# Performance work log

Measured on AMD Instinct MI355X. Metric: run time of the kernel, lower is better.

The kernel has to match this reference:

```python
import jax, jax.numpy as jnp
import numpy as np

N_NODES = 50000   # total nodes across the batch of graphs
N_EDGES = 800000  # avg degree 16
F_IN = 128        # num_features
DIM = 256         # hidden dim
N_LAYERS = 3      # num_gc_layers
N_GRAPHS = 512    # graphs in the batch (max(batch)+1)
BN_EPS = 1e-5


def setup_inputs() -> dict:
    key = jax.random.key(0)
    ks = jax.random.split(key, 16)
    inp = {}
    inp["x"] = jax.random.normal(ks[0], (N_NODES, F_IN), dtype=jnp.float32)
    inp["edge_index"] = jax.random.randint(ks[1], (2, N_EDGES), 0, N_NODES, dtype=jnp.int64)
    inp["batch"] = jnp.sort(jax.random.randint(ks[2], (N_NODES,), 0, N_GRAPHS, dtype=jnp.int64))
    k = 3
    for i in range(N_LAYERS):
        fin = F_IN if i == 0 else DIM
        inp[f"w1_{i}"] = jax.random.normal(ks[k], (fin, DIM), dtype=jnp.float32) / np.sqrt(fin); k += 1
        inp[f"b1_{i}"] = jnp.zeros((DIM,), dtype=jnp.float32)
        inp[f"w2_{i}"] = jax.random.normal(ks[k], (DIM, DIM), dtype=jnp.float32) / np.sqrt(DIM); k += 1
        inp[f"b2_{i}"] = jnp.zeros((DIM,), dtype=jnp.float32)
        inp[f"bn_g{i}"] = jnp.ones((DIM,), dtype=jnp.float32)
        inp[f"bn_b{i}"] = jnp.zeros((DIM,), dtype=jnp.float32)
    return inp


def _gin_layer(h, src, dst, w1, b1, w2, b2, g, b):
    # GINConv (eps=0): agg_i = h_i + sum_{j->i} h_j  (scatter-add over edges)
    agg = h + jax.ops.segment_sum(h[src], dst, num_segments=N_NODES)
    # MLP: Linear -> ReLU -> Linear
    m = jnp.maximum(agg @ w1 + b1, 0.0) @ w2 + b2
    # F.relu then BatchNorm1d (training mode: batch statistics, biased var)
    m = jnp.maximum(m, 0.0)
    mu = m.mean(axis=0)
    var = ((m - mu) ** 2).mean(axis=0)
    return g * (m - mu) / jnp.sqrt(var + BN_EPS) + b


def reference(x, edge_index, batch,
              w1_0, b1_0, w2_0, b2_0, bn_g0, bn_b0,
              w1_1, b1_1, w2_1, b2_1, bn_g1, bn_b1,
              w1_2, b1_2, w2_2, b2_2, bn_g2, bn_b2):
    src, dst = edge_index[0], edge_index[1]
    params = [
        (w1_0, b1_0, w2_0, b2_0, bn_g0, bn_b0),
        (w1_1, b1_1, w2_1, b2_1, bn_g1, bn_b1),
        (w1_2, b1_2, w2_2, b2_2, bn_g2, bn_b2),
    ]
    xs = []
    h = x
    for p in params:
        h = _gin_layer(h, src, dst, *p)
        xs.append(h)
    # global add-pool readout per layer, concat along feature dim
    pooled = jnp.concatenate(
        [jax.ops.segment_sum(hi, batch, num_segments=N_GRAPHS) for hi in xs], axis=1)
    return pooled, jnp.concatenate(xs, axis=1)
```

## Files before the change

kernel.cpp:

```cpp
#include <hip/hip_runtime.h>

#define N_NODES 50000
#define N_EDGES 800000
#define F_IN 128
#define DIM 256
#define N_GRAPHS 512
#define BN_EPS 1e-5f

typedef unsigned short u16;
typedef unsigned int u32;
using floatx4 = __attribute__((ext_vector_type(4))) float;
using short8 = __attribute__((ext_vector_type(8))) short;
using half2v = __attribute__((ext_vector_type(2))) _Float16;

#if __has_builtin(__builtin_amdgcn_fdot2)
#define HAS_FDOT2 1
#endif

__device__ __forceinline__ u16 f2h(float f) {
    _Float16 h = (_Float16)f;
    return __builtin_bit_cast(u16, h);
}
__device__ __forceinline__ float hlo(u32 u) {
    half2v h = __builtin_bit_cast(half2v, u);
    return (float)h.x;
}
__device__ __forceinline__ float hhi(u32 u) {
    half2v h = __builtin_bit_cast(half2v, u);
    return (float)h.y;
}
__device__ __forceinline__ u32 pack2(float a, float b) {
    half2v h = {(_Float16)a, (_Float16)b};
    return __builtin_bit_cast(u32, h);
}
__device__ __forceinline__ void dacc(u32 w, float& a, float& b) {
#ifdef HAS_FDOT2
    half2v v = __builtin_bit_cast(half2v, w);
    const half2v L = {(_Float16)1.0f, (_Float16)0.0f};
    const half2v Hm = {(_Float16)0.0f, (_Float16)1.0f};
    a = __builtin_amdgcn_fdot2(v, L, a, false);
    b = __builtin_amdgcn_fdot2(v, Hm, b, false);
#else
    a += hlo(w);
    b += hhi(w);
#endif
}
__device__ __forceinline__ void load_lds16(const void* g, void* l) {
    __builtin_amdgcn_global_load_lds((const __attribute__((address_space(1))) void*)g,
                                     (__attribute__((address_space(3))) void*)l, 16, 0, 0);
}


__global__ void count_deg(const int* __restrict__ dst, int* __restrict__ deg, int nE) {
    int e = blockIdx.x * 256 + threadIdx.x;
    if (e < nE) atomicAdd(&deg[dst[e]], 1);
}

__global__ void scan_block(const int* __restrict__ deg, int* __restrict__ row_start,
                           int* __restrict__ bsum, int n) {
    __shared__ int wtot[4];
    int i = blockIdx.x * 256 + threadIdx.x;
    int lane = threadIdx.x & 63, w = threadIdx.x >> 6;
    int v = (i < n) ? deg[i] : 0;
    int s = v;
#pragma unroll
    for (int d = 1; d < 64; d <<= 1) {
        int t = __shfl_up(s, d);
        if (lane >= d) s += t;
    }
    if (lane == 63) wtot[w] = s;
    __syncthreads();
    int off = 0;
#pragma unroll
    for (int k = 0; k < 4; ++k)
        if (k < w) off += wtot[k];
    s += off;
    if (i < n) row_start[i + 1] = s;
    if (threadIdx.x == 255) bsum[blockIdx.x] = s;
}

__global__ void scan_partials(const int* __restrict__ bsum, int* __restrict__ boff,
                              int* __restrict__ row_start, int* __restrict__ cursor, int nb) {
    __shared__ int wtot[4];
    int i = threadIdx.x;
    int lane = i & 63, w = i >> 6;
    int v = (i < nb) ? bsum[i] : 0;
    int s = v;
#pragma unroll
    for (int d = 1; d < 64; d <<= 1) {
        int t = __shfl_up(s, d);
        if (lane >= d) s += t;
    }
    if (lane == 63) wtot[w] = s;
    __syncthreads();
    int off = 0;
#pragma unroll
    for (int k = 0; k < 4; ++k)
        if (k < w) off += wtot[k];
    boff[i] = s + off - v;
    if (i == 0) { row_start[0] = 0; cursor[0] = 0; }
}

__global__ void add_offsets(int* __restrict__ row_start, int* __restrict__ cursor,
                            const int* __restrict__ boff, int n) {
    int i = blockIdx.x * 256 + threadIdx.x;
    if (i < n) {
        int fin = row_start[i + 1] + boff[blockIdx.x];
        row_start[i + 1] = fin;
        cursor[i + 1] = fin;
    }
}

__global__ void fill_csr(const int* __restrict__ src, const int* __restrict__ dst,
                         int* __restrict__ cursor, int* __restrict__ srcs, int nE) {
    int e = blockIdx.x * 256 + threadIdx.x;
    if (e < nE) {
        int p = atomicAdd(&cursor[dst[e]], 1);
        srcs[p] = src[e];
    }
}


__global__ void convert_all(const float4* __restrict__ x4, uint2* __restrict__ Hout, int n4,
                            const float* __restrict__ w10, const float* __restrict__ w11,
                            const float* __restrict__ w12, const float* __restrict__ w20,
                            const float* __restrict__ w21, const float* __restrict__ w22,
                            u16* __restrict__ Wall) {
    int i = blockIdx.x * 256 + threadIdx.x;
    if (i < n4) {
        float4 v = x4[i];
        uint2 p;
        p.x = pack2(v.x, v.y);
        p.y = pack2(v.z, v.w);
        Hout[i] = p;
        return;
    }
    int j = i - n4;
    if (j >= 360448) return;
    const float* w;
    int K, base;
    if (j < 32768)       { w = w10; K = 128; base = 0; }
    else if (j < 98304)  { w = w11; K = 256; base = 32768; }
    else if (j < 163840) { w = w12; K = 256; base = 98304; }
    else if (j < 229376) { w = w20; K = 256; base = 163840; }
    else if (j < 294912) { w = w21; K = 256; base = 229376; }
    else                 { w = w22; K = 256; base = 294912; }
    int loc = j - base;
    int nn = loc / K, kk = loc - nn * K;
    Wall[j] = f2h(w[(size_t)kk * 256 + nn]);
}


template <int K>
__global__ __launch_bounds__(256) void aggregate_v2(
    const u16* __restrict__ h, const int* __restrict__ row_start,
    const int* __restrict__ srcs, u16* __restrict__ outp, int n) {
    constexpr int RW = K / 2;
    constexpr int NSUB = (K == 256) ? 2 : 4;
    int node = (int)(((size_t)blockIdx.x * blockDim.x + threadIdx.x) >> 6);
    int lane = threadIdx.x & 63;
    if (node >= n) return;
    const u32* hb = (const u32*)h;
    const int sub = lane / (64 / NSUB);
    const int li = lane % (64 / NSUB);

    float acc[8];
#pragma unroll
    for (int t = 0; t < 8; ++t) acc[t] = 0.f;
    {
        if (sub == 0) {
            uint4 v = *(const uint4*)(hb + (size_t)node * RW + li * 4);
            dacc(v.x, acc[0], acc[1]);
            dacc(v.y, acc[2], acc[3]);
            dacc(v.z, acc[4], acc[5]);
            dacc(v.w, acc[6], acc[7]);
        }
    }

    int s = row_start[node], e = row_start[node + 1];
    for (int j0 = s; j0 < e; j0 += 64) {
        int myidx = (j0 + lane < e) ? srcs[j0 + lane] : 0;
        int cnt = min(64, e - j0);
        int j = 0;
        for (; j + NSUB * 8 - 1 < cnt; j += NSUB * 8) {
            uint4 g[8];
#pragma unroll
            for (int q = 0; q < 8; ++q) {
                int sq = __shfl(myidx, j + q * NSUB + sub);
                g[q] = *(const uint4*)(hb + (size_t)sq * RW + li * 4);
            }
#pragma unroll
            for (int q = 0; q < 8; ++q) {
                dacc(g[q].x, acc[0], acc[1]);
                dacc(g[q].y, acc[2], acc[3]);
                dacc(g[q].z, acc[4], acc[5]);
                dacc(g[q].w, acc[6], acc[7]);
            }
        }
        for (; j + NSUB * 4 - 1 < cnt; j += NSUB * 4) {
            uint4 g[4];
#pragma unroll
            for (int q = 0; q < 4; ++q) {
                int sq = __shfl(myidx, j + q * NSUB + sub);
                g[q] = *(const uint4*)(hb + (size_t)sq * RW + li * 4);
            }
#pragma unroll
            for (int q = 0; q < 4; ++q) {
                dacc(g[q].x, acc[0], acc[1]);
                dacc(g[q].y, acc[2], acc[3]);
                dacc(g[q].z, acc[4], acc[5]);
                dacc(g[q].w, acc[6], acc[7]);
            }
        }
        for (; j < cnt; j += NSUB) {
            int idx = j + sub;
            bool valid = idx < cnt;
            int sq = __shfl(myidx, valid ? idx : j);
            if (valid) {
                uint4 g = *(const uint4*)(hb + (size_t)sq * RW + li * 4);
                dacc(g.x, acc[0], acc[1]);
                dacc(g.y, acc[2], acc[3]);
                dacc(g.z, acc[4], acc[5]);
                dacc(g.w, acc[6], acc[7]);
            }
        }
    }

    if (NSUB == 4) {
#pragma unroll
        for (int t = 0; t < 8; ++t) acc[t] += __shfl_xor(acc[t], 16);
    }
#pragma unroll
    for (int t = 0; t < 8; ++t) acc[t] += __shfl_xor(acc[t], 32);

    if (sub == 0) {
        uint4 o;
        o.x = pack2(acc[0], acc[1]);
        o.y = pack2(acc[2], acc[3]);
        o.z = pack2(acc[4], acc[5]);
        o.w = pack2(acc[6], acc[7]);
        *(uint4*)((u32*)outp + (size_t)node * RW + li * 4) = o;
    }
}


template <int K1>
__global__ __launch_bounds__(512, 4) void mlp_fused(
    const u16* __restrict__ A, const u16* __restrict__ B1t, const float* __restrict__ b1,
    const u16* __restrict__ B2t, const float* __restrict__ b2,
    u16* __restrict__ Cout, float* __restrict__ sums, int M) {
    __shared__ u16 As[64 * 32];
    __shared__ u16 Bs[256 * 32];
    __shared__ u16 Ts[64 * 256];
    const int tid = threadIdx.x;
    const int w = tid >> 6, lane = tid & 63;
    const int wm = w >> 2, wn = w & 3;
    const int r = lane & 15, rg = lane >> 4;
    const int bm = blockIdx.x * 64;

    floatx4 acc[2][4];
#pragma unroll
    for (int i = 0; i < 2; ++i)
#pragma unroll
        for (int j = 0; j < 4; ++j) acc[i][j] = (floatx4){0.f, 0.f, 0.f, 0.f};

    for (int k0 = 0; k0 < K1; k0 += 32) {
        __syncthreads();
        if (tid < 256) {
            int arow = bm + (tid >> 2);
            if (arow >= M) arow = M - 1;
            load_lds16(A + (size_t)arow * K1 + k0 + (tid & 3) * 8, As + w * 512);
        }
#pragma unroll
        for (int q = 0; q < 2; ++q) {
            int i = q * 512 + tid;
            load_lds16(B1t + (size_t)(i >> 2) * K1 + k0 + (i & 3) * 8, Bs + (q * 8 + w) * 512);
        }
        __syncthreads();
        short8 a[2], b[4];
#pragma unroll
        for (int mi = 0; mi < 2; ++mi)
            a[mi] = *(const short8*)(As + (wm * 32 + mi * 16 + r) * 32 + rg * 8);
#pragma unroll
        for (int ni = 0; ni < 4; ++ni)
            b[ni] = *(const short8*)(Bs + (wn * 64 + ni * 16 + r) * 32 + rg * 8);
#pragma unroll
        for (int mi = 0; mi < 2; ++mi)
#pragma unroll
            for (int ni = 0; ni < 4; ++ni)
                acc[mi][ni] = __builtin_amdgcn_mfma_f32_16x16x32_f16(a[mi], b[ni], acc[mi][ni], 0, 0, 0);
    }
#pragma unroll
    for (int ni = 0; ni < 4; ++ni) {
        int col = wn * 64 + ni * 16 + r;
        float bv = b1[col];
#pragma unroll
        for (int mi = 0; mi < 2; ++mi)
#pragma unroll
            for (int rr = 0; rr < 4; ++rr) {
                int lrow = wm * 32 + mi * 16 + rg * 4 + rr;
                float v = fmaxf(acc[mi][ni][rr] + bv, 0.f);
                int chunk = (col >> 3) ^ (lrow & 7);
                *(u16*)((char*)Ts + lrow * 512 + chunk * 16 + (col & 7) * 2) = f2h(v);
            }
#pragma unroll
        for (int mi = 0; mi < 2; ++mi) acc[mi][ni] = (floatx4){0.f, 0.f, 0.f, 0.f};
    }

    for (int k0 = 0; k0 < 256; k0 += 32) {
        __syncthreads();
#pragma unroll
        for (int q = 0; q < 2; ++q) {
            int i = q * 512 + tid;
            load_lds16(B2t + (size_t)(i >> 2) * 256 + k0 + (i & 3) * 8, Bs + (q * 8 + w) * 512);
        }
        __syncthreads();
        short8 a[2], b[4];
#pragma unroll
        for (int mi = 0; mi < 2; ++mi) {
            int lrow = wm * 32 + mi * 16 + r;
            int chunk = ((k0 >> 3) + rg) ^ (lrow & 7);
            a[mi] = *(const short8*)((const char*)Ts + lrow * 512 + chunk * 16);
        }
#pragma unroll
        for (int ni = 0; ni < 4; ++ni)
            b[ni] = *(const short8*)(Bs + (wn * 64 + ni * 16 + r) * 32 + rg * 8);
#pragma unroll
        for (int mi = 0; mi < 2; ++mi)
#pragma unroll
            for (int ni = 0; ni < 4; ++ni)
                acc[mi][ni] = __builtin_amdgcn_mfma_f32_16x16x32_f16(a[mi], b[ni], acc[mi][ni], 0, 0, 0);
    }

#pragma unroll
    for (int ni = 0; ni < 4; ++ni) {
        int col = wn * 64 + ni * 16 + r;
        float bv = b2[col];
        float s = 0.f, s2 = 0.f;
#pragma unroll
        for (int mi = 0; mi < 2; ++mi)
#pragma unroll
            for (int rr = 0; rr < 4; ++rr) {
                int row = bm + wm * 32 + mi * 16 + rg * 4 + rr;
                if (row < M) {
                    float v = fmaxf(acc[mi][ni][rr] + bv, 0.f);
                    u16 qb = f2h(v);
                    float vq = hlo((u32)qb);
                    Cout[(size_t)row * 256 + col] = qb;
                    s += vq;
                    s2 += vq * vq;
                }
            }
        s += __shfl_xor(s, 16);
        s += __shfl_xor(s, 32);
        s2 += __shfl_xor(s2, 16);
        s2 += __shfl_xor(s2, 32);
        if (rg == 0) {
            atomicAdd(&sums[col], s);
            atomicAdd(&sums[256 + col], s2);
        }
    }
}


template <int WRITE_H>
__global__ void bn_apply_pool(const u16* __restrict__ Mb, const float* __restrict__ sums,
                              const float* __restrict__ g, const float* __restrict__ bb,
                              const int* __restrict__ batch, float* __restrict__ out_nodes,
                              u16* __restrict__ H, float* __restrict__ pooled,
                              int col_off, int n, float inv_n) {
    int w = threadIdx.x >> 6, lane = threadIdx.x & 63;
    int base = blockIdx.x * 64 + w * 16;
    if (base >= n) return;
    int c4 = lane << 2;
    float4 s1 = *(const float4*)(sums + c4);
    float4 s2 = *(const float4*)(sums + 256 + c4);
    float4 g4 = *(const float4*)(g + c4);
    float4 b4 = *(const float4*)(bb + c4);
    float4 sc, sh;
    {
        float mux = s1.x * inv_n, muy = s1.y * inv_n, muz = s1.z * inv_n, muw = s1.w * inv_n;
        sc.x = g4.x / sqrtf(s2.x * inv_n - mux * mux + BN_EPS);
        sc.y = g4.y / sqrtf(s2.y * inv_n - muy * muy + BN_EPS);
        sc.z = g4.z / sqrtf(s2.z * inv_n - muz * muz + BN_EPS);
        sc.w = g4.w / sqrtf(s2.w * inv_n - muw * muw + BN_EPS);
        sh.x = b4.x - mux * sc.x;
        sh.y = b4.y - muy * sc.y;
        sh.z = b4.z - muz * sc.z;
        sh.w = b4.w - muw * sc.w;
    }
    float4 acc = make_float4(0.f, 0.f, 0.f, 0.f);
    int gcur = -1;
    int end = min(base + 16, n);
    for (int row = base; row < end; ++row) {
        uint2 pk = *(const uint2*)(Mb + (size_t)row * 256 + c4);
        float4 o;
        o.x = fmaf(hlo(pk.x), sc.x, sh.x);
        o.y = fmaf(hhi(pk.x), sc.y, sh.y);
        o.z = fmaf(hlo(pk.y), sc.z, sh.z);
        o.w = fmaf(hhi(pk.y), sc.w, sh.w);
        floatx4 ov = {o.x, o.y, o.z, o.w};
        __builtin_nontemporal_store(ov, (floatx4*)(out_nodes + (size_t)row * 768 + col_off + c4));
        if (WRITE_H) {
            uint2 hk;
            hk.x = pack2(o.x, o.y);
            hk.y = pack2(o.z, o.w);
            *(uint2*)(H + (size_t)row * 256 + c4) = hk;
        }
        int gg = batch[row];
        if (gg != gcur) {
            if (gcur >= 0) {
                float* pp = pooled + (size_t)gcur * 768 + col_off + c4;
                atomicAdd(pp + 0, acc.x);
                atomicAdd(pp + 1, acc.y);
                atomicAdd(pp + 2, acc.z);
                atomicAdd(pp + 3, acc.w);
            }
            gcur = gg;
            acc = o;
        } else {
            acc.x += o.x; acc.y += o.y; acc.z += o.z; acc.w += o.w;
        }
    }
    if (gcur >= 0) {
        float* pp = pooled + (size_t)gcur * 768 + col_off + c4;
        atomicAdd(pp + 0, acc.x);
        atomicAdd(pp + 1, acc.y);
        atomicAdd(pp + 2, acc.z);
        atomicAdd(pp + 3, acc.w);
    }
}


extern "C" void kernel_launch(void* const* d_in, const int* in_sizes, int n_in,
                              void* d_out, int out_size, void* d_ws, size_t ws_size,
                              hipStream_t stream) {
    const float* x = (const float*)d_in[0];
    const int* esrc = (const int*)d_in[1];
    const int* edst = esrc + N_EDGES;
    const int* batch = (const int*)d_in[2];

    const float* w1[3] = {(const float*)d_in[3], (const float*)d_in[9], (const float*)d_in[15]};
    const float* b1[3] = {(const float*)d_in[4], (const float*)d_in[10], (const float*)d_in[16]};
    const float* w2[3] = {(const float*)d_in[5], (const float*)d_in[11], (const float*)d_in[17]};
    const float* b2[3] = {(const float*)d_in[6], (const float*)d_in[12], (const float*)d_in[18]};
    const float* bng[3] = {(const float*)d_in[7], (const float*)d_in[13], (const float*)d_in[19]};
    const float* bnb[3] = {(const float*)d_in[8], (const float*)d_in[14], (const float*)d_in[20]};

    float* out_pooled = (float*)d_out;
    float* out_nodes = (float*)d_out + (size_t)N_GRAPHS * 768;

    char* p = (char*)d_ws;
    u16* Abf = (u16*)p; p += (size_t)N_NODES * 256 * 2;
    u16* Mb = (u16*)p;  p += (size_t)N_NODES * 256 * 2;
    u16* H = (u16*)p;   p += (size_t)N_NODES * 256 * 2;
    u16* Wall = (u16*)p; p += (size_t)360448 * 2;
    float* sums = (float*)p; p += 3 * 512 * 4;
    int* deg = (int*)p;      p += (size_t)N_NODES * 4;
    const size_t zero_bytes = 3 * 512 * 4 + (size_t)N_NODES * 4;
    int* row_start = (int*)p; p += (size_t)(N_NODES + 1) * 4;
    int* cursor = (int*)p;    p += (size_t)(N_NODES + 1) * 4;
    int* srcs = (int*)p;      p += (size_t)N_EDGES * 4;
    int* bsum = (int*)p;      p += 256 * 4;
    int* boff = (int*)p;      p += 256 * 4;

    const u16* W1t[3] = {Wall, Wall + 32768, Wall + 98304};
    const u16* W2t[3] = {Wall + 163840, Wall + 229376, Wall + 294912};

    const int NBLK = (N_NODES + 255) / 256;

    hipMemsetAsync(sums, 0, zero_bytes, stream);
    hipMemsetAsync(out_pooled, 0, (size_t)N_GRAPHS * 768 * sizeof(float), stream);

    count_deg<<<(N_EDGES + 255) / 256, 256, 0, stream>>>(edst, deg, N_EDGES);
    scan_block<<<NBLK, 256, 0, stream>>>(deg, row_start, bsum, N_NODES);
    scan_partials<<<1, 256, 0, stream>>>(bsum, boff, row_start, cursor, NBLK);
    add_offsets<<<NBLK, 256, 0, stream>>>(row_start, cursor, boff, N_NODES);
    fill_csr<<<(N_EDGES + 255) / 256, 256, 0, stream>>>(esrc, edst, cursor, srcs, N_EDGES);

    {
        const int n4 = N_NODES * F_IN / 4;
        const int tot = n4 + 360448;
        convert_all<<<(tot + 255) / 256, 256, 0, stream>>>(
            (const float4*)x, (uint2*)H, n4,
            w1[0], w1[1], w1[2], w2[0], w2[1], w2[2], Wall);
    }

    const int AGRID = (N_NODES + 3) / 4;
    const int MGRID = (N_NODES + 63) / 64;
    const int PBLK = (N_NODES + 63) / 64;
    for (int L = 0; L < 3; ++L) {
        float* sumsL = sums + L * 512;
        if (L == 0) {
            aggregate_v2<128><<<AGRID, 256, 0, stream>>>(H, row_start, srcs, Abf, N_NODES);
            mlp_fused<128><<<MGRID, 512, 0, stream>>>(Abf, W1t[L], b1[L], W2t[L], b2[L],
                                                      Mb, sumsL, N_NODES);
        } else {
            aggregate_v2<256><<<AGRID, 256, 0, stream>>>(H, row_start, srcs, Abf, N_NODES);
            mlp_fused<256><<<MGRID, 512, 0, stream>>>(Abf, W1t[L], b1[L], W2t[L], b2[L],
                                                      Mb, sumsL, N_NODES);
        }
        if (L < 2)
            bn_apply_pool<1><<<PBLK, 256, 0, stream>>>(Mb, sumsL, bng[L], bnb[L], batch,
                                                       out_nodes, H, out_pooled, L * 256, N_NODES, 1.0f / N_NODES);
        else
            bn_apply_pool<0><<<PBLK, 256, 0, stream>>>(Mb, sumsL, bng[L], bnb[L], batch,
                                                       out_nodes, H, out_pooled, L * 256, N_NODES, 1.0f / N_NODES);
    }
}
```

Measured before the change: 703.2 us.

## Fold BatchNorm affine into next-layer aggregation and widen MLP K-tile to 64

The next layer's aggregation now gathers the raw pre-BN fp16 MLP output and applies the BatchNorm scale and shift after summing, using the fact that BN is per-feature affine (scale*sum + (deg+1)*shift). This removes the separate fp16 H write from the BN/pool kernel, which becomes a plain bn_pool that only writes outputs and pooled sums. The fused MLP kernel also doubles its K-step to 64 with XOR-swizzled LDS tiles, which halves the barrier count. In exchange it uses more LDS, so launch bounds drop to 2 blocks per SM. Summing un-normalised values in fp16 and applying the affine afterwards may change rounding slightly.

```diff
diff --git a/kernel.cpp b/kernel.cpp
--- a/kernel.cpp
+++ b/kernel.cpp
@@ -151,10 +151,12 @@
 }
 
 
-template <int K>
+template <int K, int AFFINE>
 __global__ __launch_bounds__(256) void aggregate_v2(
     const u16* __restrict__ h, const int* __restrict__ row_start,
-    const int* __restrict__ srcs, u16* __restrict__ outp, int n) {
+    const int* __restrict__ srcs, u16* __restrict__ outp,
+    const float* __restrict__ sums, const float* __restrict__ g,
+    const float* __restrict__ bb, float inv_n, int n) {
     constexpr int RW = K / 2;
     constexpr int NSUB = (K == 256) ? 2 : 4;
     int node = (int)(((size_t)blockIdx.x * blockDim.x + threadIdx.x) >> 6);
@@ -183,33 +185,33 @@
         int cnt = min(64, e - j0);
         int j = 0;
         for (; j + NSUB * 8 - 1 < cnt; j += NSUB * 8) {
-            uint4 g[8];
+            uint4 gg[8];
 #pragma unroll
             for (int q = 0; q < 8; ++q) {
                 int sq = __shfl(myidx, j + q * NSUB + sub);
-                g[q] = *(const uint4*)(hb + (size_t)sq * RW + li * 4);
+                gg[q] = *(const uint4*)(hb + (size_t)sq * RW + li * 4);
             }
 #pragma unroll
             for (int q = 0; q < 8; ++q) {
-                dacc(g[q].x, acc[0], acc[1]);
-                dacc(g[q].y, acc[2], acc[3]);
-                dacc(g[q].z, acc[4], acc[5]);
-                dacc(g[q].w, acc[6], acc[7]);
+                dacc(gg[q].x, acc[0], acc[1]);
+                dacc(gg[q].y, acc[2], acc[3]);
+                dacc(gg[q].z, acc[4], acc[5]);
+                dacc(gg[q].w, acc[6], acc[7]);
             }
         }
         for (; j + NSUB * 4 - 1 < cnt; j += NSUB * 4) {
-            uint4 g[4];
+            uint4 gg[4];
 #pragma unroll
             for (int q = 0; q < 4; ++q) {
                 int sq = __shfl(myidx, j + q * NSUB + sub);
-                g[q] = *(const uint4*)(hb + (size_t)sq * RW + li * 4);
+                gg[q] = *(const uint4*)(hb + (size_t)sq * RW + li * 4);
             }
 #pragma unroll
             for (int q = 0; q < 4; ++q) {
-                dacc(g[q].x, acc[0], acc[1]);
-                dacc(g[q].y, acc[2], acc[3]);
-                dacc(g[q].z, acc[4], acc[5]);
-                dacc(g[q].w, acc[6], acc[7]);
+                dacc(gg[q].x, acc[0], acc[1]);
+                dacc(gg[q].y, acc[2], acc[3]);
+                dacc(gg[q].z, acc[4], acc[5]);
+                dacc(gg[q].w, acc[6], acc[7]);
             }
         }
         for (; j < cnt; j += NSUB) {
@@ -217,11 +219,11 @@
             bool valid = idx < cnt;
             int sq = __shfl(myidx, valid ? idx : j);
             if (valid) {
-                uint4 g = *(const uint4*)(hb + (size_t)sq * RW + li * 4);
-                dacc(g.x, acc[0], acc[1]);
-                dacc(g.y, acc[2], acc[3]);
-                dacc(g.z, acc[4], acc[5]);
-                dacc(g.w, acc[6], acc[7]);
+                uint4 gg = *(const uint4*)(hb + (size_t)sq * RW + li * 4);
+                dacc(gg.x, acc[0], acc[1]);
+                dacc(gg.y, acc[2], acc[3]);
+                dacc(gg.z, acc[4], acc[5]);
+                dacc(gg.w, acc[6], acc[7]);
             }
         }
     }
@@ -234,6 +236,25 @@
     for (int t = 0; t < 8; ++t) acc[t] += __shfl_xor(acc[t], 32);
 
     if (sub == 0) {
+        if (AFFINE) {
+            int c = li * 8;
+            float degp1 = (float)(e - s + 1);
+            float4 s1a = *(const float4*)(sums + c), s1b = *(const float4*)(sums + c + 4);
+            float4 s2a = *(const float4*)(sums + 256 + c), s2b = *(const float4*)(sums + 256 + c + 4);
+            float4 g4a = *(const float4*)(g + c), g4b = *(const float4*)(g + c + 4);
+            float4 b4a = *(const float4*)(bb + c), b4b = *(const float4*)(bb + c + 4);
+            float mu[8] = {s1a.x, s1a.y, s1a.z, s1a.w, s1b.x, s1b.y, s1b.z, s1b.w};
+            float q2[8] = {s2a.x, s2a.y, s2a.z, s2a.w, s2b.x, s2b.y, s2b.z, s2b.w};
+            float gv[8] = {g4a.x, g4a.y, g4a.z, g4a.w, g4b.x, g4b.y, g4b.z, g4b.w};
+            float bv[8] = {b4a.x, b4a.y, b4a.z, b4a.w, b4b.x, b4b.y, b4b.z, b4b.w};
+#pragma unroll
+            for (int t = 0; t < 8; ++t) {
+                float m = mu[t] * inv_n;
+                float sc = gv[t] / sqrtf(q2[t] * inv_n - m * m + BN_EPS);
+                float sh = bv[t] - m * sc;
+                acc[t] = sc * acc[t] + degp1 * sh;
+            }
+        }
         uint4 o;
         o.x = pack2(acc[0], acc[1]);
         o.y = pack2(acc[2], acc[3]);
@@ -245,12 +266,12 @@
 
 
 template <int K1>
-__global__ __launch_bounds__(512, 4) void mlp_fused(
+__global__ __launch_bounds__(512, 2) void mlp_fused(
     const u16* __restrict__ A, const u16* __restrict__ B1t, const float* __restrict__ b1,
     const u16* __restrict__ B2t, const float* __restrict__ b2,
     u16* __restrict__ Cout, float* __restrict__ sums, int M) {
-    __shared__ u16 As[64 * 32];
-    __shared__ u16 Bs[256 * 32];
+    __shared__ u16 As[64 * 64];
+    __shared__ u16 Bs[256 * 64];
     __shared__ u16 Ts[64 * 256];
     const int tid = threadIdx.x;
     const int w = tid >> 6, lane = tid & 63;
@@ -264,31 +285,48 @@
 #pragma unroll
         for (int j = 0; j < 4; ++j) acc[i][j] = (floatx4){0.f, 0.f, 0.f, 0.f};
 
-    for (int k0 = 0; k0 < K1; k0 += 32) {
+    for (int k0 = 0; k0 < K1; k0 += 64) {
         __syncthreads();
-        if (tid < 256) {
-            int arow = bm + (tid >> 2);
+        {
+            int arow = bm + (tid >> 3);
             if (arow >= M) arow = M - 1;
-            load_lds16(A + (size_t)arow * K1 + k0 + (tid & 3) * 8, As + w * 512);
-        }
-#pragma unroll
-        for (int q = 0; q < 2; ++q) {
+            int swz = (tid & 7) ^ ((tid >> 3) & 7);
+            load_lds16(A + (size_t)arow * K1 + k0 + swz * 8, As + w * 512);
+        }
+#pragma unroll
+        for (int q = 0; q < 4; ++q) {
             int i = q * 512 + tid;
-            load_lds16(B1t + (size_t)(i >> 2) * K1 + k0 + (i & 3) * 8, Bs + (q * 8 + w) * 512);
+            int nrow = i >> 3;
+            int swz = (i & 7) ^ (nrow & 7);
+            load_lds16(B1t + (size_t)nrow * K1 + k0 + swz * 8, Bs + q * 4096 + w * 512);
         }
         __syncthreads();
-        short8 a[2], b[4];
-#pragma unroll
-        for (int mi = 0; mi < 2; ++mi)
-            a[mi] = *(const short8*)(As + (wm * 32 + mi * 16 + r) * 32 + rg * 8);
-#pragma unroll
-        for (int ni = 0; ni < 4; ++ni)
-            b[ni] = *(const short8*)(Bs + (wn * 64 + ni * 16 + r) * 32 + rg * 8);
-#pragma unroll
-        for (int mi = 0; mi < 2; ++mi)
-#pragma unroll
-            for (int ni = 0; ni < 4; ++ni)
-                acc[mi][ni] = __builtin_amdgcn_mfma_f32_16x16x32_f16(a[mi], b[ni], acc[mi][ni], 0, 0, 0);
+        short8 a[2][2], b[4][2];
+#pragma unroll
+        for (int mi = 0; mi < 2; ++mi) {
+            int row = wm * 32 + mi * 16 + r;
+#pragma unroll
+            for (int kk = 0; kk < 2; ++kk) {
+                int ck = (kk * 4 + rg) ^ (row & 7);
+                a[mi][kk] = *(const short8*)(As + row * 64 + ck * 8);
+            }
+        }
+#pragma unroll
+        for (int ni = 0; ni < 4; ++ni) {
+            int row = wn * 64 + ni * 16 + r;
+#pragma unroll
+            for (int kk = 0; kk < 2; ++kk) {
+                int ck = (kk * 4 + rg) ^ (row & 7);
+                b[ni][kk] = *(const short8*)(Bs + row * 64 + ck * 8);
+            }
+        }
+#pragma unroll
+        for (int kk = 0; kk < 2; ++kk)
+#pragma unroll
+            for (int mi = 0; mi < 2; ++mi)
+#pragma unroll
+                for (int ni = 0; ni < 4; ++ni)
+                    acc[mi][ni] = __builtin_amdgcn_mfma_f32_16x16x32_f16(a[mi][kk], b[ni][kk], acc[mi][ni], 0, 0, 0);
     }
 #pragma unroll
     for (int ni = 0; ni < 4; ++ni) {
@@ -307,29 +345,42 @@
         for (int mi = 0; mi < 2; ++mi) acc[mi][ni] = (floatx4){0.f, 0.f, 0.f, 0.f};
     }
 
-    for (int k0 = 0; k0 < 256; k0 += 32) {
+    for (int k0 = 0; k0 < 256; k0 += 64) {
         __syncthreads();
 #pragma unroll
-        for (int q = 0; q < 2; ++q) {
+        for (int q = 0; q < 4; ++q) {
             int i = q * 512 + tid;
-            load_lds16(B2t + (size_t)(i >> 2) * 256 + k0 + (i & 3) * 8, Bs + (q * 8 + w) * 512);
+            int nrow = i >> 3;
+            int swz = (i & 7) ^ (nrow & 7);
+            load_lds16(B2t + (size_t)nrow * 256 + k0 + swz * 8, Bs + q * 4096 + w * 512);
         }
         __syncthreads();
-        short8 a[2], b[4];
+        short8 a[2][2], b[4][2];
 #pragma unroll
         for (int mi = 0; mi < 2; ++mi) {
             int lrow = wm * 32 + mi * 16 + r;
-            int chunk = ((k0 >> 3) + rg) ^ (lrow & 7);
-            a[mi] = *(const short8*)((const char*)Ts + lrow * 512 + chunk * 16);
-        }
-#pragma unroll
-        for (int ni = 0; ni < 4; ++ni)
-            b[ni] = *(const short8*)(Bs + (wn * 64 + ni * 16 + r) * 32 + rg * 8);
-#pragma unroll
-        for (int mi = 0; mi < 2; ++mi)
-#pragma unroll
-            for (int ni = 0; ni < 4; ++ni)
-                acc[mi][ni] = __builtin_amdgcn_mfma_f32_16x16x32_f16(a[mi], b[ni], acc[mi][ni], 0, 0, 0);
+#pragma unroll
+            for (int kk = 0; kk < 2; ++kk) {
+                int ck = ((k0 >> 3) + kk * 4 + rg) ^ (lrow & 7);
+                a[mi][kk] = *(const short8*)((const char*)Ts + lrow * 512 + ck * 16);
+            }
+        }
+#pragma unroll
+        for (int ni = 0; ni < 4; ++ni) {
+            int row = wn * 64 + ni * 16 + r;
+#pragma unroll
+            for (int kk = 0; kk < 2; ++kk) {
+                int ck = (kk * 4 + rg) ^ (row & 7);
+                b[ni][kk] = *(const short8*)(Bs + row * 64 + ck * 8);
+            }
+        }
+#pragma unroll
+        for (int kk = 0; kk < 2; ++kk)
+#pragma unroll
+            for (int mi = 0; mi < 2; ++mi)
+#pragma unroll
+                for (int ni = 0; ni < 4; ++ni)
+                    acc[mi][ni] = __builtin_amdgcn_mfma_f32_16x16x32_f16(a[mi][kk], b[ni][kk], acc[mi][ni], 0, 0, 0);
     }
 
 #pragma unroll
@@ -363,12 +414,10 @@
 }
 
 
-template <int WRITE_H>
-__global__ void bn_apply_pool(const u16* __restrict__ Mb, const float* __restrict__ sums,
-                              const float* __restrict__ g, const float* __restrict__ bb,
-                              const int* __restrict__ batch, float* __restrict__ out_nodes,
-                              u16* __restrict__ H, float* __restrict__ pooled,
-                              int col_off, int n, float inv_n) {
+__global__ void bn_pool(const u16* __restrict__ Mb, const float* __restrict__ sums,
+                        const float* __restrict__ g, const float* __restrict__ bb,
+                        const int* __restrict__ batch, float* __restrict__ out_nodes,
+                        float* __restrict__ pooled, int col_off, int n, float inv_n) {
     int w = threadIdx.x >> 6, lane = threadIdx.x & 63;
     int base = blockIdx.x * 64 + w * 16;
     if (base >= n) return;
@@ -401,12 +450,6 @@
         o.w = fmaf(hhi(pk.y), sc.w, sh.w);
         floatx4 ov = {o.x, o.y, o.z, o.w};
         __builtin_nontemporal_store(ov, (floatx4*)(out_nodes + (size_t)row * 768 + col_off + c4));
-        if (WRITE_H) {
-            uint2 hk;
-            hk.x = pack2(o.x, o.y);
-            hk.y = pack2(o.z, o.w);
-            *(uint2*)(H + (size_t)row * 256 + c4) = hk;
-        }
         int gg = batch[row];
         if (gg != gcur) {
             if (gcur >= 0) {
@@ -489,22 +532,21 @@
     const int AGRID = (N_NODES + 3) / 4;
     const int MGRID = (N_NODES + 63) / 64;
     const int PBLK = (N_NODES + 63) / 64;
-    for (int L = 0; L < 3; ++L) {
-        float* sumsL = sums + L * 512;
-        if (L == 0) {
-            aggregate_v2<128><<<AGRID, 256, 0, stream>>>(H, row_start, srcs, Abf, N_NODES);
-            mlp_fused<128><<<MGRID, 512, 0, stream>>>(Abf, W1t[L], b1[L], W2t[L], b2[L],
-                                                      Mb, sumsL, N_NODES);
-        } else {
-            aggregate_v2<256><<<AGRID, 256, 0, stream>>>(H, row_start, srcs, Abf, N_NODES);
-            mlp_fused<256><<<MGRID, 512, 0, stream>>>(Abf, W1t[L], b1[L], W2t[L], b2[L],
-                                                      Mb, sumsL, N_NODES);
-        }
-        if (L < 2)
-            bn_apply_pool<1><<<PBLK, 256, 0, stream>>>(Mb, sumsL, bng[L], bnb[L], batch,
-                                                       out_nodes, H, out_pooled, L * 256, N_NODES, 1.0f / N_NODES);
-        else
-            bn_apply_pool<0><<<PBLK, 256, 0, stream>>>(Mb, sumsL, bng[L], bnb[L], batch,
-                                                       out_nodes, H, out_pooled, L * 256, N_NODES, 1.0f / N_NODES);
-    }
-}
+    const float inv_n = 1.0f / N_NODES;
+
+    aggregate_v2<128, 0><<<AGRID, 256, 0, stream>>>(H, row_start, srcs, Abf,
+                                                    nullptr, nullptr, nullptr, inv_n, N_NODES);
+    mlp_fused<128><<<MGRID, 512, 0, stream>>>(Abf, W1t[0], b1[0], W2t[0], b2[0], Mb, sums, N_NODES);
+    aggregate_v2<256, 1><<<AGRID, 256, 0, stream>>>(Mb, row_start, srcs, Abf,
+                                                    sums, bng[0], bnb[0], inv_n, N_NODES);
+    bn_pool<<<PBLK, 256, 0, stream>>>(Mb, sums, bng[0], bnb[0], batch, out_nodes, out_pooled,
+                                      0, N_NODES, inv_n);
+    mlp_fused<256><<<MGRID, 512, 0, stream>>>(Abf, W1t[1], b1[1], W2t[1], b2[1], Mb, sums + 512, N_NODES);
+    aggregate_v2<256, 1><<<AGRID, 256, 0, stream>>>(Mb, row_start, srcs, Abf,
+                                                    sums + 512, bng[1], bnb[1], inv_n, N_NODES);
+    bn_pool<<<PBLK, 256, 0, stream>>>(Mb, sums + 512, bng[1], bnb[1], batch, out_nodes, out_pooled,
+                                      256, N_NODES, inv_n);
+    mlp_fused<256><<<MGRID, 512, 0, stream>>>(Abf, W1t[2], b1[2], W2t[2], b2[2], Mb, sums + 1024, N_NODES);
+    bn_pool<<<PBLK, 256, 0, stream>>>(Mb, sums + 1024, bng[2], bnb[2], batch, out_nodes, out_pooled,
+                                      512, N_NODES, inv_n);
+}
```

New measurement: 695.8 us. Within noise of the previous version (-1.1%).
